# Kernel optimization log

Measured on AMD Instinct MI355X. Metric: run time of the kernel, lower is better.

Reference implementation:

```python
import jax, jax.numpy as jnp
from jax import lax
import numpy as np

OUTS = [5, 1, 2, 2, 1, 1, 1, 1]  # heatmap, conf, dxy, wh, dist, offset, severity, surface
OFFS = np.concatenate([[0], np.cumsum(OUTS)])
BN_EPS = 1e-5


def setup_inputs() -> dict:
    key = jax.random.key(0)
    ks = jax.random.split(key, 10)
    N, C, Hf, Wf = 16, 576, 12, 20
    f = jax.random.normal(ks[0], (N, C, Hf, Wf), jnp.float32)
    det_w1 = jax.random.normal(ks[1], (8, C, C, 3, 3), jnp.float32) * 0.02
    det_bn_g = 1.0 + 0.1 * jax.random.normal(ks[2], (8, C), jnp.float32)
    det_bn_b = 0.1 * jax.random.normal(ks[3], (8, C), jnp.float32)
    det_bn_m = 0.1 * jax.random.normal(ks[4], (8, C), jnp.float32)
    det_bn_v = jax.random.uniform(ks[5], (8, C), jnp.float32) + 0.5
    det_w2 = jax.random.normal(ks[6], (14, C), jnp.float32) * 0.05
    det_b2 = jax.random.normal(ks[7], (14,), jnp.float32) * 0.05
    lin_W = jax.random.normal(ks[8], (10, C), jnp.float32) * 0.05
    lin_b = jnp.zeros((10,), jnp.float32)
    return dict(f=f, det_w1=det_w1, det_bn_g=det_bn_g, det_bn_b=det_bn_b,
                det_bn_m=det_bn_m, det_bn_v=det_bn_v, det_w2=det_w2, det_b2=det_b2,
                lin_W=lin_W, lin_b=lin_b, frame_w=640, frame_h=384)


def _head(f, w1, g, b, m, v, w2, b2):
    # conv3x3 (no bias) -> BN (inference) -> SiLU -> conv1x1
    dn = ('NCHW', 'OIHW', 'NCHW')
    h = lax.conv_general_dilated(f, w1, (1, 1), 'SAME', dimension_numbers=dn)
    scale = g * lax.rsqrt(v + BN_EPS)
    h = h * scale[None, :, None, None] + (b - m * scale)[None, :, None, None]
    h = h * jax.nn.sigmoid(h)  # SiLU
    return jnp.einsum('nchw,oc->nohw', h, w2) + b2[None, :, None, None]


def _forward(f, det_w1, det_bn_g, det_bn_b, det_bn_m, det_bn_v, det_w2, det_b2,
             lin_W, lin_b, frame_w, frame_h, max_dets=20):
    N, C, Hf, Wf = f.shape
    eps = 1e-5
    # ---- legacy single-hazard head from pooled features ----
    f1 = f.mean(axis=(2, 3))                      # [N, 576]  (AdaptiveAvgPool2d(1))
    lin = f1 @ lin_W.T + lin_b                    # [N, 10]
    conf = jnp.clip(jax.nn.sigmoid(lin[:, 0:1]), eps, 1.0 - eps)
    type_log = lin[:, 1:6]
    dist_m = jax.nn.sigmoid(lin[:, 6:7]) * 3.0
    offset = jnp.tanh(lin[:, 7:8])
    severity = jnp.clip(jax.nn.sigmoid(lin[:, 8:9]), eps, 1.0 - eps)
    surface = jnp.clip(jax.nn.sigmoid(lin[:, 9:10]), eps, 1.0 - eps)
    type_id = jnp.argmax(type_log, axis=1, keepdims=True).astype(f.dtype)
    single_out = jnp.concatenate([conf, type_id, dist_m, offset, severity, surface], axis=1)

    # ---- dense per-pixel heads ----
    maps = []
    for i in range(8):
        o0, o1 = int(OFFS[i]), int(OFFS[i + 1])
        maps.append(_head(f, det_w1[i], det_bn_g[i], det_bn_b[i],
                          det_bn_m[i], det_bn_v[i], det_w2[o0:o1], det_b2[o0:o1]))
    heat = jax.nn.sigmoid(maps[0])                # [N,5,H,W]
    conf_d = jax.nn.sigmoid(maps[1])              # [N,1,H,W]
    dxy = jax.nn.sigmoid(maps[2])                 # [N,2,H,W]
    wh = jax.nn.sigmoid(maps[3])                  # [N,2,H,W]
    dist = jax.nn.sigmoid(maps[4]) * 3.0          # [N,1,H,W]
    offsm = jnp.tanh(maps[5])
    sev = jax.nn.sigmoid(maps[6])
    surf = jax.nn.sigmoid(maps[7])

    # ---- per-class topk decode ----
    score_flat = (conf_d * heat).reshape(N, 5, Hf * Wf)
    k = min(max_dets, Hf * Wf)
    topk_scores, topk_idx = lax.top_k(score_flat, k)          # [N,5,k]
    top_scores = topk_scores.reshape(N, -1)                    # [N,5k]
    top_class = jnp.broadcast_to(jnp.arange(5, dtype=f.dtype)[None, :, None], (N, 5, k)).reshape(N, -1)
    idx_flat = topk_idx.reshape(N, -1)                          # [N,5k]
    y_idx = (idx_flat // Wf).astype(f.dtype)
    x_idx = (idx_flat % Wf).astype(f.dtype)

    g1 = lambda m: jnp.take_along_axis(m.reshape(N, -1), idx_flat, axis=1)
    gx, gy = g1(dxy[:, 0]), g1(dxy[:, 1])
    gw, gh = g1(wh[:, 0]), g1(wh[:, 1])
    gdist, goffs = g1(dist), g1(offsm)
    gsev, gsurf = g1(sev), g1(surf)

    stride_x = frame_w / Wf
    stride_y = frame_h / Hf
    cx = jnp.clip(x_idx + gx, 0, Wf - 1) * stride_x
    cy = jnp.clip(y_idx + gy, 0, Hf - 1) * stride_y
    bw = jnp.clip(gw, 0, 1) * frame_w
    bh = jnp.clip(gh, 0, 1) * frame_h
    x1 = jnp.clip(cx - bw / 2, 0, frame_w - 1)
    y1 = jnp.clip(cy - bh / 2, 0, frame_h - 1)
    x2 = jnp.clip(cx + bw / 2, 0, frame_w - 1)
    y2 = jnp.clip(cy + bh / 2, 0, frame_h - 1)

    dets = jnp.stack([top_scores, top_class, gdist, goffs, gsev, gsurf, x1, y1, x2, y2], axis=-1)  # [N,5k,10]
    order = jnp.argsort(dets[:, :, 2], axis=-1)   # ascending distance (nearest first)
    dets_sorted = jnp.take_along_axis(dets, order[:, :, None], axis=1)
    dets_out = dets_sorted[:, :max_dets, :]        # [N,K,10]
    return single_out, dets_out


def reference(f, det_w1, det_bn_g, det_bn_b, det_bn_m, det_bn_v, det_w2, det_b2,
              lin_W, lin_b, frame_w, frame_h):
    return _forward(f, det_w1, det_bn_g, det_bn_b, det_bn_m, det_bn_v,
                    det_w2, det_b2, lin_W, lin_b, frame_w, frame_h)
```

## Files before the change

### kernel.cpp

```cpp
#include <hip/hip_runtime.h>
#include <math.h>

#define NB 16
#define CC 576
#define HH 12
#define WW 20
#define PP 240
#define MM 3840
#define NHEAD 8
#define HALO 22

typedef __attribute__((ext_vector_type(8))) short short8;
typedef __attribute__((ext_vector_type(4))) float floatx4;
typedef unsigned short ushort_t;

__device__ __forceinline__ float sigmoidf_(float x) {
    return 1.0f / (1.0f + expf(-x));
}
__device__ __forceinline__ unsigned short f2bf(float x) {
    union { float f; unsigned u; } v; v.f = x;
    unsigned r = v.u + 0x7fff + ((v.u >> 16) & 1);
    return (unsigned short)(r >> 16);
}
__device__ __forceinline__ float bf2f(unsigned short b) {
    union { float f; unsigned u; } v; v.u = ((unsigned)b) << 16;
    return v.f;
}

__global__ __launch_bounds__(256) void k_single(const float* __restrict__ f1sum,
                                                const float* __restrict__ linW,
                                                const float* __restrict__ linb,
                                                float* __restrict__ out) {
    int n = blockIdx.x;
    __shared__ float lin[10];
    int t = threadIdx.x;
    int lane = t & 63, wave = t >> 6;
    const float inv = 1.0f / PP;
    for (int o = wave; o < 10; o += 4) {
        const float* wrow = linW + o * CC;
        float s = 0.f;
        for (int c = lane; c < CC; c += 64)
            s = fmaf(f1sum[n * CC + c] * inv, wrow[c], s);
        #pragma unroll
        for (int off = 32; off; off >>= 1) s += __shfl_xor(s, off, 64);
        if (lane == 0) lin[o] = s + linb[o];
    }
    __syncthreads();
    if (t == 0) {
        const float eps = 1e-5f;
        float conf = sigmoidf_(lin[0]);
        conf = fminf(fmaxf(conf, eps), 1.f - eps);
        int best = 0; float bv = lin[1];
        #pragma unroll
        for (int j = 1; j < 5; ++j) { if (lin[1 + j] > bv) { bv = lin[1 + j]; best = j; } }
        float dist = 3.f * sigmoidf_(lin[6]);
        float offs = tanhf(lin[7]);
        float sev  = fminf(fmaxf(sigmoidf_(lin[8]), eps), 1.f - eps);
        float surf = fminf(fmaxf(sigmoidf_(lin[9]), eps), 1.f - eps);
        float* o = out + n * 6;
        o[0] = conf; o[1] = (float)best; o[2] = dist;
        o[3] = offs; o[4] = sev; o[5] = surf;
    }
}

__global__ __launch_bounds__(256) void k_prep_f(const float* __restrict__ f,
                                                ushort_t* __restrict__ fhi,
                                                ushort_t* __restrict__ flo,
                                                float* __restrict__ f1sum) {
    __shared__ float tile[32][33];
    int c0 = blockIdx.x * 32, p0 = blockIdx.y * 32, n = blockIdx.z;
    int tp = threadIdx.x & 31, tc8 = threadIdx.x >> 5;
    for (int cc = tc8; cc < 32; cc += 8) {
        int p = p0 + tp;
        tile[cc][tp] = (p < PP) ? f[((size_t)n * CC + c0 + cc) * PP + p] : 0.f;
    }
    __syncthreads();
    if (threadIdx.x < 32) {
        float s = 0.f;
        #pragma unroll
        for (int pp = 0; pp < 32; ++pp) s += tile[threadIdx.x][pp];
        atomicAdd(&f1sum[n * CC + c0 + threadIdx.x], s);
    }
    int tcw = threadIdx.x & 31, tpw = threadIdx.x >> 5;
    for (int pp = tpw; pp < 32; pp += 8) {
        int p = p0 + pp;
        if (p < PP) {
            float v = tile[tcw][pp];
            unsigned short hi = f2bf(v);
            size_t o = ((size_t)n * PP + p) * CC + c0 + tcw;
            fhi[o] = hi;
            flo[o] = f2bf(v - bf2f(hi));
        }
    }
}

__global__ __launch_bounds__(256) void k_prep_w(const float* __restrict__ w1,
                                                ushort_t* __restrict__ whi,
                                                ushort_t* __restrict__ wlo) {
    __shared__ float ws[CC * 9];
    int co = blockIdx.x % CC;
    int h  = blockIdx.x / CC;
    const float* src = w1 + ((size_t)(h * CC + co)) * CC * 9;
    for (int i = threadIdx.x; i < CC * 9 / 4; i += 256)
        *(float4*)(ws + i * 4) = *(const float4*)(src + i * 4);
    __syncthreads();
    for (int idx = threadIdx.x; idx < 9 * 72; idx += 256) {
        int tap = idx / 72, pos = idx - tap * 72;
        short8 vh, vl;
        #pragma unroll
        for (int e = 0; e < 8; ++e) {
            float v = ws[(pos * 8 + e) * 9 + tap];
            unsigned short hi = f2bf(v);
            vh[e] = (short)hi;
            vl[e] = (short)f2bf(v - bf2f(hi));
        }
        size_t ob = ((size_t)(h * 9 + tap) * CC + co) * CC + (size_t)pos * 8;
        *(short8*)(whi + ob) = vh;
        *(short8*)(wlo + ob) = vl;
    }
}

__global__ __launch_bounds__(256) void k_conv_mfma(
        const ushort_t* __restrict__ fhi, const ushort_t* __restrict__ flo,
        const ushort_t* __restrict__ whi, const ushort_t* __restrict__ wlo,
        const float* __restrict__ w2,
        const float* __restrict__ bng, const float* __restrict__ bnb,
        const float* __restrict__ bnm, const float* __restrict__ bnv,
        float* __restrict__ maps) {
    __shared__ __align__(16) ushort_t Ah[1216 * 8];
    __shared__ __align__(16) ushort_t Al[1216 * 8];
    __shared__ __align__(16) ushort_t Bh[256 * 8];
    __shared__ __align__(16) ushort_t Bl[256 * 8];
    __shared__ ushort_t rowmap[9 * 256];

    int t = threadIdx.x;

    int bid = blockIdx.x;
    int xcd = bid & 7;
    int q = bid >> 3;
    int mt = q % 15;
    int slice = (q / 15) * 8 + xcd;
    int m0 = mt * 256;
    int c0 = (slice % 9) * 64;
    int h  = slice / 9;

    int w = t >> 6, lane = t & 63;
    int quad = lane >> 4, l15 = lane & 15;
    int srow_lo = t & 15, sg = (t >> 4) & 3, srb = t >> 6;

    int bco = srb * 16 + srow_lo;
    size_t bconst = (size_t)(c0 + bco) * CC + sg * 8;
    const size_t hbase = (size_t)h * 9 * CC * CC;

    short8 pbh, pbl;
    {
        size_t src = hbase + bconst;
        pbh = *(const short8*)(whi + src);
        pbl = *(const short8*)(wlo + src);
    }

    if (t < 32) {
        int arr = t >> 4, g = (t >> 2) & 3, rr = 12 + (t & 3);
        int idx = 18 * 64 + g * 16 + rr;
        short8 z = {0, 0, 0, 0, 0, 0, 0, 0};
        *(short8*)((arr ? Al : Ah) + idx * 8) = z;
    }
    for (int idx = t; idx < 9 * 256; idx += 256) {
        int tap = idx >> 8, ml = idx & 255;
        int m = m0 + ml;
        int p = m % PP;
        int y = p / WW, x = p - y * WW;
        int dy = tap / 3 - 1, dx = tap % 3 - 1;
        int yy = y + dy, xx = x + dx;
        int row;
        if ((unsigned)yy < (unsigned)HH && (unsigned)xx < (unsigned)WW)
            row = ml + dy * WW + dx + HALO;
        else
            row = 300 + (ml & 3);
        rowmap[idx] = (ushort_t)row;
    }
    __syncthreads();

    floatx4 acc[4][4];
    #pragma unroll
    for (int i = 0; i < 4; ++i)
        #pragma unroll
        for (int j = 0; j < 4; ++j) acc[i][j] = (floatx4){0.f, 0.f, 0.f, 0.f};

    for (int cib = 0; cib < 18; ++cib) {
        __syncthreads();
        int koff = cib * 32 + sg * 8;
        #pragma unroll
        for (int it = 0; it < 5; ++it) {
            int row = (srb + 4 * it) * 16 + srow_lo;
            if (row < 300) {
                int mg = m0 - HALO + row;
                int cidx = 256 * it + t;
                short8 vh = {0, 0, 0, 0, 0, 0, 0, 0};
                short8 vl = {0, 0, 0, 0, 0, 0, 0, 0};
                if ((unsigned)mg < (unsigned)MM) {
                    vh = *(const short8*)(fhi + (size_t)mg * CC + koff);
                    vl = *(const short8*)(flo + (size_t)mg * CC + koff);
                }
                *(short8*)(Ah + cidx * 8) = vh;
                *(short8*)(Al + cidx * 8) = vl;
            }
        }
        for (int tap = 0; tap < 9; ++tap) {
            if (tap) __syncthreads();
            {
                *(short8*)(Bh + t * 8) = pbh;
                *(short8*)(Bl + t * 8) = pbl;
            }
            if (cib * 9 + tap + 1 < 162) {
                int ncib = (tap == 8) ? cib + 1 : cib;
                int ntap = (tap == 8) ? 0 : tap + 1;
                size_t src = hbase + (size_t)ntap * (CC * CC) + bconst
                           + (size_t)ncib * 32;
                pbh = *(const short8*)(whi + src);
                pbl = *(const short8*)(wlo + src);
            }
            __syncthreads();

            short8 bh[4], bl[4], ah[4], al[4];
            #pragma unroll
            for (int j = 0; j < 4; ++j) {
                bh[j] = *(const short8*)(Bh + (j * 64 + lane) * 8);
                bl[j] = *(const short8*)(Bl + (j * 64 + lane) * 8);
            }
            #pragma unroll
            for (int i = 0; i < 4; ++i) {
                int r = rowmap[tap * 256 + w * 64 + i * 16 + l15];
                int a16 = ((r >> 4) * 64 + quad * 16 + (r & 15)) * 8;
                ah[i] = *(const short8*)(Ah + a16);
                al[i] = *(const short8*)(Al + a16);
            }
            #pragma unroll
            for (int i = 0; i < 4; ++i)
                #pragma unroll
                for (int j = 0; j < 4; ++j)
                    acc[i][j] = __builtin_amdgcn_mfma_f32_16x16x32_bf16(
                        ah[i], bh[j], acc[i][j], 0, 0, 0);
            #pragma unroll
            for (int i = 0; i < 4; ++i)
                #pragma unroll
                for (int j = 0; j < 4; ++j)
                    acc[i][j] = __builtin_amdgcn_mfma_f32_16x16x32_bf16(
                        ah[i], bl[j], acc[i][j], 0, 0, 0);
            #pragma unroll
            for (int i = 0; i < 4; ++i)
                #pragma unroll
                for (int j = 0; j < 4; ++j)
                    acc[i][j] = __builtin_amdgcn_mfma_f32_16x16x32_bf16(
                        al[i], bh[j], acc[i][j], 0, 0, 0);
        }
    }

    float scale[4], shift[4];
    #pragma unroll
    for (int j = 0; j < 4; ++j) {
        int c = h * CC + c0 + j * 16 + l15;
        float g_ = bng[c], bb = bnb[c], bm = bnm[c], bv = bnv[c];
        scale[j] = g_ / sqrtf(bv + 1e-5f);
        shift[j] = bb - bm * scale[j];
    }
    #pragma unroll
    for (int i = 0; i < 4; ++i)
        #pragma unroll
        for (int j = 0; j < 4; ++j)
            #pragma unroll
            for (int r = 0; r < 4; ++r) {
                float hx = fmaf(acc[i][j][r], scale[j], shift[j]);
                acc[i][j][r] = hx * sigmoidf_(hx);
            }

    static const int OFFo[NHEAD + 1] = {0, 5, 6, 8, 10, 11, 12, 13, 14};
    int o0 = OFFo[h], o1 = OFFo[h + 1];
    for (int o = o0; o < o1; ++o) {
        float w2v[4];
        #pragma unroll
        for (int j = 0; j < 4; ++j) w2v[j] = w2[o * CC + c0 + j * 16 + l15];
        float pv[4][4];
        #pragma unroll
        for (int i = 0; i < 4; ++i)
            #pragma unroll
            for (int r = 0; r < 4; ++r) {
                float s = 0.f;
                #pragma unroll
                for (int j = 0; j < 4; ++j) s = fmaf(acc[i][j][r], w2v[j], s);
                pv[i][r] = s;
            }
        #pragma unroll
        for (int off = 1; off < 16; off <<= 1)
            #pragma unroll
            for (int i = 0; i < 4; ++i)
                #pragma unroll
                for (int r = 0; r < 4; ++r)
                    pv[i][r] += __shfl_xor(pv[i][r], off, 64);
        if (l15 == 0) {
            #pragma unroll
            for (int i = 0; i < 4; ++i)
                #pragma unroll
                for (int r = 0; r < 4; ++r) {
                    int m = m0 + w * 64 + i * 16 + quad * 4 + r;
                    int n = m / PP, p = m - n * PP;
                    atomicAdd(&maps[(n * 14 + o) * PP + p], pv[i][r]);
                }
        }
    }
}

__global__ __launch_bounds__(256) void k_decode(
        const float* __restrict__ maps,
        const float* __restrict__ b2,
        const int* __restrict__ fw_p, const int* __restrict__ fh_p,
        float* __restrict__ out) {
    int n = blockIdx.x;
    int t = threadIdx.x;
    __shared__ float ms[14][PP];
    __shared__ float sconf[PP];
    __shared__ float cscore[100];
    __shared__ int   cidx[100];
    __shared__ float dets[100][10];
    __shared__ float dvals[100];

    const float* mp = maps + (size_t)n * 14 * PP;
    for (int idx = t; idx < 14 * PP; idx += 256)
        ms[idx / PP][idx % PP] = mp[idx] + b2[idx / PP];
    __syncthreads();
    if (t < PP) sconf[t] = sigmoidf_(ms[5][t]);
    __syncthreads();

    int wv = t >> 6, lane = t & 63;
    for (int cls = wv; cls < 5; cls += 4) {
        float v[4]; int pi[4];
        #pragma unroll
        for (int j = 0; j < 4; ++j) {
            int p = lane + 64 * j;
            pi[j] = p;
            v[j] = (p < PP) ? sconf[p] * sigmoidf_(ms[cls][p]) : -1e30f;
        }
        for (int r = 0; r < 20; ++r) {
            float bv = v[0]; int bi = pi[0];
            #pragma unroll
            for (int j = 1; j < 4; ++j)
                if (v[j] > bv || (v[j] == bv && pi[j] < bi)) { bv = v[j]; bi = pi[j]; }
            float rv = bv; int ri = bi;
            #pragma unroll
            for (int off = 32; off; off >>= 1) {
                float ov = __shfl_xor(rv, off, 64);
                int   oi = __shfl_xor(ri, off, 64);
                if (ov > rv || (ov == rv && oi < ri)) { rv = ov; ri = oi; }
            }
            if (lane == 0) { cscore[cls * 20 + r] = rv; cidx[cls * 20 + r] = ri; }
            #pragma unroll
            for (int j = 0; j < 4; ++j) if (pi[j] == ri) v[j] = -1e30f;
        }
    }
    __syncthreads();

    if (t < 100) {
        int cls = t / 20;
        int p = cidx[t];
        int yi = p / WW, xi = p - yi * WW;
        float gx = sigmoidf_(ms[6][p]),  gy = sigmoidf_(ms[7][p]);
        float gw = sigmoidf_(ms[8][p]),  gh = sigmoidf_(ms[9][p]);
        float gd = 3.f * sigmoidf_(ms[10][p]);
        float go = tanhf(ms[11][p]);
        float gs = sigmoidf_(ms[12][p]);
        float gf = sigmoidf_(ms[13][p]);
        float fw = (float)fw_p[0], fh = (float)fh_p[0];
        float sx = fw / (float)WW, sy = fh / (float)HH;
        float cx = fminf(fmaxf((float)xi + gx, 0.f), (float)WW - 1.f) * sx;
        float cy = fminf(fmaxf((float)yi + gy, 0.f), (float)HH - 1.f) * sy;
        float bw = fminf(fmaxf(gw, 0.f), 1.f) * fw;
        float bh = fminf(fmaxf(gh, 0.f), 1.f) * fh;
        float x1 = fminf(fmaxf(cx - bw * 0.5f, 0.f), fw - 1.f);
        float y1 = fminf(fmaxf(cy - bh * 0.5f, 0.f), fh - 1.f);
        float x2 = fminf(fmaxf(cx + bw * 0.5f, 0.f), fw - 1.f);
        float y2 = fminf(fmaxf(cy + bh * 0.5f, 0.f), fh - 1.f);
        dets[t][0] = cscore[t]; dets[t][1] = (float)cls;
        dets[t][2] = gd; dets[t][3] = go; dets[t][4] = gs; dets[t][5] = gf;
        dets[t][6] = x1; dets[t][7] = y1; dets[t][8] = x2; dets[t][9] = y2;
        dvals[t] = gd;
    }
    __syncthreads();
    if (t < 100) {
        float d = dvals[t];
        int rank = 0;
        for (int l = 0; l < 100; ++l) {
            float dl = dvals[l];
            rank += (dl < d) || (dl == d && l < t);
        }
        if (rank < 20) {
            float* o = out + 96 + ((size_t)n * 20 + rank) * 10;
            #pragma unroll
            for (int q = 0; q < 10; ++q) o[q] = dets[t][q];
        }
    }
}

extern "C" void kernel_launch(void* const* d_in, const int* in_sizes, int n_in,
                              void* d_out, int out_size, void* d_ws, size_t ws_size,
                              hipStream_t stream) {
    const float* f    = (const float*)d_in[0];
    const float* w1   = (const float*)d_in[1];
    const float* bng  = (const float*)d_in[2];
    const float* bnb  = (const float*)d_in[3];
    const float* bnm  = (const float*)d_in[4];
    const float* bnv  = (const float*)d_in[5];
    const float* w2   = (const float*)d_in[6];
    const float* b2   = (const float*)d_in[7];
    const float* linW = (const float*)d_in[8];
    const float* linb = (const float*)d_in[9];
    const int*   fw   = (const int*)d_in[10];
    const int*   fh   = (const int*)d_in[11];
    float* out = (float*)d_out;

    const size_t w_elems = (size_t)NHEAD * 9 * CC * CC;
    const size_t f_elems = (size_t)MM * CC;

    ushort_t* ws_whi = (ushort_t*)d_ws;
    ushort_t* ws_wlo = ws_whi + w_elems;
    ushort_t* ws_fhi = ws_wlo + w_elems;
    ushort_t* ws_flo = ws_fhi + f_elems;
    float*    ws_maps = (float*)(ws_flo + f_elems);
    float*    ws_f1sum = (float*)d_ws;

    hipMemsetAsync(ws_f1sum, 0, (size_t)NB * CC * sizeof(float), stream);
    hipMemsetAsync(ws_maps, 0, (size_t)NB * 14 * PP * sizeof(float), stream);
    k_prep_f<<<dim3(CC / 32, (PP + 31) / 32, NB), 256, 0, stream>>>(
        f, ws_fhi, ws_flo, ws_f1sum);
    k_single<<<NB, 256, 0, stream>>>(ws_f1sum, linW, linb, out);
    k_prep_w<<<NHEAD * CC, 256, 0, stream>>>(w1, ws_whi, ws_wlo);
    k_conv_mfma<<<dim3(15 * 9 * NHEAD), 256, 0, stream>>>(
        ws_fhi, ws_flo, ws_whi, ws_wlo, w2, bng, bnb, bnm, bnv, ws_maps);
    k_decode<<<NB, 256, 0, stream>>>(ws_maps, b2, fw, fh, out);
}
```

Baseline: 731.1 us.

## Pre-swizzle weights into MFMA fragment order and load B directly to registers

```diff
diff --git a/kernel.cpp b/kernel.cpp
--- a/kernel.cpp
+++ b/kernel.cpp
@@ -97,30 +97,42 @@
 __global__ __launch_bounds__(256) void k_prep_w(const float* __restrict__ w1,
                                                 ushort_t* __restrict__ whi,
                                                 ushort_t* __restrict__ wlo) {
-    __shared__ float ws[CC * 9];
-    int co = blockIdx.x % CC;
-    int h  = blockIdx.x / CC;
-    const float* src = w1 + ((size_t)(h * CC + co)) * CC * 9;
-    for (int i = threadIdx.x; i < CC * 9 / 4; i += 256)
-        *(float4*)(ws + i * 4) = *(const float4*)(src + i * 4);
-    __syncthreads();
-    for (int idx = threadIdx.x; idx < 9 * 72; idx += 256) {
-        int tap = idx / 72, pos = idx - tap * 72;
+    __shared__ float ws[288 * 33];
+    int b = blockIdx.x;
+    int cib = b % 18;
+    int rest = b / 18;
+    int half = rest & 1;
+    int hc = rest >> 1;
+    int t = threadIdx.x;
+    const float* src = w1
+        + ((size_t)(hc / 9) * CC + (hc % 9) * 64 + half * 32) * (CC * 9)
+        + (size_t)cib * 288;
+    for (int i = t; i < 32 * 288; i += 256) {
+        int co = i / 288, k = i - co * 288;
+        ws[k * 33 + co] = src[(size_t)co * (CC * 9) + k];
+    }
+    __syncthreads();
+    size_t obase = ((size_t)hc * 18 + cib) * 18432 + (size_t)half * 1024;
+    for (int idx = t; idx < 9 * 2 * 64; idx += 256) {
+        int tap = idx / 128, r = idx - tap * 128;
+        int jj = r >> 6, lane = r & 63;
+        int col = jj * 16 + (lane & 15);
+        int krow = (lane >> 4) * 8;
         short8 vh, vl;
         #pragma unroll
         for (int e = 0; e < 8; ++e) {
-            float v = ws[(pos * 8 + e) * 9 + tap];
+            float v = ws[((krow + e) * 9 + tap) * 33 + col];
             unsigned short hi = f2bf(v);
             vh[e] = (short)hi;
             vl[e] = (short)f2bf(v - bf2f(hi));
         }
-        size_t ob = ((size_t)(h * 9 + tap) * CC + co) * CC + (size_t)pos * 8;
-        *(short8*)(whi + ob) = vh;
-        *(short8*)(wlo + ob) = vl;
-    }
-}
-
-__global__ __launch_bounds__(256) void k_conv_mfma(
+        size_t o = obase + (size_t)tap * 2048 + jj * 512 + lane * 8;
+        *(short8*)(whi + o) = vh;
+        *(short8*)(wlo + o) = vl;
+    }
+}
+
+__global__ __launch_bounds__(256, 3) void k_conv_mfma(
         const ushort_t* __restrict__ fhi, const ushort_t* __restrict__ flo,
         const ushort_t* __restrict__ whi, const ushort_t* __restrict__ wlo,
         const float* __restrict__ w2,
@@ -129,8 +141,6 @@
         float* __restrict__ maps) {
     __shared__ __align__(16) ushort_t Ah[1216 * 8];
     __shared__ __align__(16) ushort_t Al[1216 * 8];
-    __shared__ __align__(16) ushort_t Bh[256 * 8];
-    __shared__ __align__(16) ushort_t Bl[256 * 8];
     __shared__ ushort_t rowmap[9 * 256];
 
     int t = threadIdx.x;
@@ -141,22 +151,22 @@
     int mt = q % 15;
     int slice = (q / 15) * 8 + xcd;
     int m0 = mt * 256;
-    int c0 = (slice % 9) * 64;
+    int c0b = slice % 9;
+    int c0 = c0b * 64;
     int h  = slice / 9;
 
     int w = t >> 6, lane = t & 63;
     int quad = lane >> 4, l15 = lane & 15;
     int srow_lo = t & 15, sg = (t >> 4) & 3, srb = t >> 6;
 
-    int bco = srb * 16 + srow_lo;
-    size_t bconst = (size_t)(c0 + bco) * CC + sg * 8;
-    const size_t hbase = (size_t)h * 9 * CC * CC;
-
-    short8 pbh, pbl;
-    {
-        size_t src = hbase + bconst;
-        pbh = *(const short8*)(whi + src);
-        pbl = *(const short8*)(wlo + src);
+    const ushort_t* bp_h = whi + (size_t)(h * 9 + c0b) * 331776 + lane * 8;
+    const ushort_t* bp_l = wlo + (size_t)(h * 9 + c0b) * 331776 + lane * 8;
+
+    short8 cbh[4], cbl[4];
+    #pragma unroll
+    for (int j = 0; j < 4; ++j) {
+        cbh[j] = *(const short8*)(bp_h + j * 512);
+        cbl[j] = *(const short8*)(bp_l + j * 512);
     }
 
     if (t < 32) {
@@ -206,28 +216,22 @@
                 *(short8*)(Al + cidx * 8) = vl;
             }
         }
+        __syncthreads();
         for (int tap = 0; tap < 9; ++tap) {
-            if (tap) __syncthreads();
-            {
-                *(short8*)(Bh + t * 8) = pbh;
-                *(short8*)(Bl + t * 8) = pbl;
-            }
-            if (cib * 9 + tap + 1 < 162) {
-                int ncib = (tap == 8) ? cib + 1 : cib;
-                int ntap = (tap == 8) ? 0 : tap + 1;
-                size_t src = hbase + (size_t)ntap * (CC * CC) + bconst
-                           + (size_t)ncib * 32;
-                pbh = *(const short8*)(whi + src);
-                pbl = *(const short8*)(wlo + src);
-            }
-            __syncthreads();
-
-            short8 bh[4], bl[4], ah[4], al[4];
-            #pragma unroll
-            for (int j = 0; j < 4; ++j) {
-                bh[j] = *(const short8*)(Bh + (j * 64 + lane) * 8);
-                bl[j] = *(const short8*)(Bl + (j * 64 + lane) * 8);
-            }
+            int step = cib * 9 + tap;
+            short8 nbh[4], nbl[4];
+            if (step < 161) {
+                int nt = tap + 1, nc = cib;
+                if (nt == 9) { nt = 0; ++nc; }
+                size_t o = (size_t)nc * 18432 + (size_t)nt * 2048;
+                #pragma unroll
+                for (int j = 0; j < 4; ++j) {
+                    nbh[j] = *(const short8*)(bp_h + o + j * 512);
+                    nbl[j] = *(const short8*)(bp_l + o + j * 512);
+                }
+            }
+
+            short8 ah[4], al[4];
             #pragma unroll
             for (int i = 0; i < 4; ++i) {
                 int r = rowmap[tap * 256 + w * 64 + i * 16 + l15];
@@ -238,21 +242,18 @@
             #pragma unroll
             for (int i = 0; i < 4; ++i)
                 #pragma unroll
-                for (int j = 0; j < 4; ++j)
+                for (int j = 0; j < 4; ++j) {
                     acc[i][j] = __builtin_amdgcn_mfma_f32_16x16x32_bf16(
-                        ah[i], bh[j], acc[i][j], 0, 0, 0);
-            #pragma unroll
-            for (int i = 0; i < 4; ++i)
-                #pragma unroll
-                for (int j = 0; j < 4; ++j)
+                        ah[i], cbh[j], acc[i][j], 0, 0, 0);
                     acc[i][j] = __builtin_amdgcn_mfma_f32_16x16x32_bf16(
-                        ah[i], bl[j], acc[i][j], 0, 0, 0);
-            #pragma unroll
-            for (int i = 0; i < 4; ++i)
-                #pragma unroll
-                for (int j = 0; j < 4; ++j)
+                        ah[i], cbl[j], acc[i][j], 0, 0, 0);
                     acc[i][j] = __builtin_amdgcn_mfma_f32_16x16x32_bf16(
-                        al[i], bh[j], acc[i][j], 0, 0, 0);
+                        al[i], cbh[j], acc[i][j], 0, 0, 0);
+                }
+            if (step < 161) {
+                #pragma unroll
+                for (int j = 0; j < 4; ++j) { cbh[j] = nbh[j]; cbl[j] = nbl[j]; }
+            }
         }
     }
 
@@ -432,7 +433,7 @@
     k_prep_f<<<dim3(CC / 32, (PP + 31) / 32, NB), 256, 0, stream>>>(
         f, ws_fhi, ws_flo, ws_f1sum);
     k_single<<<NB, 256, 0, stream>>>(ws_f1sum, linW, linb, out);
-    k_prep_w<<<NHEAD * CC, 256, 0, stream>>>(w1, ws_whi, ws_wlo);
+    k_prep_w<<<NHEAD * 9 * 2 * 18, 256, 0, stream>>>(w1, ws_whi, ws_wlo);
     k_conv_mfma<<<dim3(15 * 9 * NHEAD), 256, 0, stream>>>(
         ws_fhi, ws_flo, ws_whi, ws_wlo, w2, bng, bnb, bnm, bnv, ws_maps);
     k_decode<<<NB, 256, 0, stream>>>(ws_maps, b2, fw, fh, out);
```

Result: no change. 730.6 us (-0.1%).
